# Kernel tuning notes

Measured on AMD Instinct MI355X. Metric: run time of the kernel, lower is better.

## Reference

```python
import jax, jax.numpy as jnp
import numpy as np

D_MODEL = 768
N_HEAD = 12


def setup_inputs() -> dict:
    key = jax.random.key(0)
    k1, k2, k3, k4, k5 = jax.random.split(key, 5)
    B, T, C = 4, 2048, D_MODEL
    s = 1.0 / np.sqrt(C)
    return {
        "x": jax.random.normal(k1, (B, T, C), dtype=jnp.float32),
        "w_attn": jax.random.normal(k2, (C, 3 * C), dtype=jnp.float32) * s,
        "b_attn": jax.random.normal(k3, (3 * C,), dtype=jnp.float32) * 0.02,
        "w_proj": jax.random.normal(k4, (C, C), dtype=jnp.float32) * s,
        "b_proj": jax.random.normal(k5, (C,), dtype=jnp.float32) * 0.02,
    }


def reference(x, w_attn, b_attn, w_proj, b_proj):
    B, T, C = x.shape
    H = N_HEAD
    Dh = C // H
    qkv = x @ w_attn + b_attn                      # [B, T, 3C]
    q, k, v = jnp.split(qkv, 3, axis=-1)
    # [B, H, T, Dh]
    q = q.reshape(B, T, H, Dh).transpose(0, 2, 1, 3)
    k = k.reshape(B, T, H, Dh).transpose(0, 2, 1, 3)
    v = v.reshape(B, T, H, Dh).transpose(0, 2, 1, 3)
    att = jnp.einsum("bhqd,bhkd->bhqk", q, k) * (1.0 / np.sqrt(Dh))
    causal = jnp.tril(jnp.ones((T, T), dtype=bool))
    att = jnp.where(causal[None, None, :, :], att, -jnp.inf)
    att = jax.nn.softmax(att, axis=-1)             # dropout p=0 (eval)
    y = jnp.einsum("bhqk,bhkd->bhqd", att, v)      # [B, H, T, Dh]
    y = y.transpose(0, 2, 1, 3).reshape(B, T, C)
    return y @ w_proj + b_proj
```

## Files before the change

### kernel.cpp

```cpp
#include <hip/hip_runtime.h>
#include <stdint.h>

#define NHEAD 12
#define DH 64
#define BATCH 4
#define SEQ 2048
#define CDIM 768
#define MROWS (BATCH*SEQ)

typedef __attribute__((ext_vector_type(8))) short short8;
typedef __attribute__((ext_vector_type(4))) float floatx4;
typedef unsigned int u32;

__device__ inline unsigned short f2bf(float f) {
    union { float f; unsigned u; } v; v.f = f;
    unsigned r = v.u + 0x7FFFu + ((v.u >> 16) & 1u);
    return (unsigned short)(r >> 16);
}

__device__ __forceinline__ u32 pk_bf16(float a, float b) {
    u32 d;
    asm("v_cvt_pk_bf16_f32 %0, %1, %2" : "=v"(d) : "v"(a), "v"(b));
    return d;
}

__device__ __forceinline__ void async_cp16(const unsigned short* g, unsigned short* l) {
    __builtin_amdgcn_global_load_lds(
        (const __attribute__((address_space(1))) u32*)g,
        (__attribute__((address_space(3))) u32*)l, 16, 0, 0);
}

template<int N> __device__ __forceinline__ void waitcnt_vm() {
    if constexpr (N == 0)      asm volatile("s_waitcnt vmcnt(0)" ::: "memory");
    else if constexpr (N == 3) asm volatile("s_waitcnt vmcnt(3)" ::: "memory");
    else if constexpr (N == 4) asm volatile("s_waitcnt vmcnt(4)" ::: "memory");
}

__device__ __forceinline__ void transpose_tile(
    const float* __restrict__ in, unsigned short* __restrict__ out,
    int K, int N, int k0, int n0, unsigned short (*T)[72]) {
    const int t = threadIdx.x;
    const int nc = t & 63, kw = t >> 6;
    for (int i = 0; i < 16; i++) {
        const int kr = kw + i * 4;
        T[nc][kr] = f2bf(in[(size_t)(k0 + kr) * N + n0 + nc]);
    }
    __syncthreads();
    const int row = t >> 2, seg = t & 3;
    uint4 a = *(const uint4*)&T[row][seg * 16];
    uint4 b2 = *(const uint4*)&T[row][seg * 16 + 8];
    unsigned short* o = &out[(size_t)(n0 + row) * K + k0 + seg * 16];
    *(uint4*)o = a;
    *(uint4*)(o + 8) = b2;
}

__global__ __launch_bounds__(256) void prep_kernel(
    const float* __restrict__ x,      unsigned short* __restrict__ xb,
    const float* __restrict__ wa,     unsigned short* __restrict__ wta,
    const float* __restrict__ wp,     unsigned short* __restrict__ wtp) {
    __shared__ unsigned short T[64][72];
    const int lin = blockIdx.x;
    if (lin < 6144) {
        const int i = (lin * 256 + threadIdx.x) * 4;
        float4 f = *(const float4*)(x + i);
        union { unsigned short s[4]; uint2 u; } p;
        p.s[0] = f2bf(f.x); p.s[1] = f2bf(f.y);
        p.s[2] = f2bf(f.z); p.s[3] = f2bf(f.w);
        *(uint2*)(xb + i) = p.u;
    } else if (lin < 6144 + 432) {
        const int t2 = lin - 6144;
        transpose_tile(wa, wta, CDIM, 3 * CDIM, (t2 % 12) * 64, (t2 / 12) * 64, T);
    } else {
        const int t3 = lin - 6576;
        transpose_tile(wp, wtp, CDIM, CDIM, (t3 % 12) * 64, (t3 / 12) * 64, T);
    }
}

template<int MODE, int KD, int BM, int BN>
__global__ __launch_bounds__(256) void gemm_bf16(
    const unsigned short* __restrict__ A,
    const unsigned short* __restrict__ BT,
    const float* __restrict__ bias,
    float* __restrict__ Cout,
    unsigned short* __restrict__ Qout,
    unsigned short* __restrict__ Kout,
    unsigned short* __restrict__ VTout,
    int Ndim)
{
    constexpr int TM = BM / 32, TN = BN / 32;
    constexpr int CHA = BM / 64, CHB = BN / 64;
    __shared__ unsigned short SH[3 * (BM + BN) * 32];
    auto As = [&](int b3) { return &SH[b3 * BM * 32]; };
    auto Bs = [&](int b3) { return &SH[3 * BM * 32 + b3 * BN * 32]; };

    const int tid  = threadIdx.x;
    const int wave = tid >> 6;
    const int lane = tid & 63;
    const int l16  = lane & 15;
    const int quad = lane >> 4;
    const int wm = wave >> 1, wn = wave & 1;
    const int m0 = blockIdx.x * BM;
    const int n0 = blockIdx.y * BN;

    const int rloc = lane >> 2;
    const int gs   = (((lane & 3) ^ (rloc & 3) ^ ((rloc >> 2) & 3))) * 8;
    const int pg   = ((quad ^ (l16 & 3) ^ ((l16 >> 2) & 3))) * 8;

    floatx4 acc[TM][TN];
    for (int i = 0; i < TM; i++)
        for (int j = 0; j < TN; j++) acc[i][j] = (floatx4)0.0f;

    constexpr int NIT = KD / 32;

    auto stageTo = [&](int s, int buf) {
        const int koff = s * 32;
        for (int ch = 0; ch < CHA; ch++) {
            const int row = wave * CHA * 16 + ch * 16 + rloc;
            async_cp16(&A[(size_t)(m0 + row) * KD + koff + gs],
                       &As(buf)[(wave * CHA + ch) * 512]);
        }
        for (int ch = 0; ch < CHB; ch++) {
            const int row = wave * CHB * 16 + ch * 16 + rloc;
            async_cp16(&BT[(size_t)(n0 + row) * KD + koff + gs],
                       &Bs(buf)[(wave * CHB + ch) * 512]);
        }
    };
    stageTo(0, 0);
    stageTo(1, 1);

    int buf = 0;
    for (int it = 0; it < NIT; it++) {
        if (it < NIT - 1) waitcnt_vm<CHA + CHB>();
        else              waitcnt_vm<0>();
        asm volatile("s_barrier" ::: "memory");
        if (it + 2 < NIT) {
            int b2 = buf + 2; if (b2 >= 3) b2 -= 3;
            stageTo(it + 2, b2);
        }
        short8 a[TM], b[TN];
        for (int i = 0; i < TM; i++)
            a[i] = *(const short8*)&As(buf)[(wm * (BM / 2) + i * 16 + l16) * 32 + pg];
        for (int j = 0; j < TN; j++)
            b[j] = *(const short8*)&Bs(buf)[(wn * (BN / 2) + j * 16 + l16) * 32 + pg];
        for (int i = 0; i < TM; i++)
            for (int j = 0; j < TN; j++)
                acc[i][j] = __builtin_amdgcn_mfma_f32_16x16x32_bf16(
                    a[i], b[j], acc[i][j], 0, 0, 0);
        buf++; if (buf >= 3) buf = 0;
    }

    const float QSCALE = 0.18033688011112042f;

    if (MODE == 1 && (n0 / CDIM) == 2) {
        __syncthreads();
        unsigned short* scr = &SH[wave * (64 * 68)];
        for (int i = 0; i < TM; i++) {
            const int tl = i * 16 + quad * 4;
            for (int j = 0; j < TN; j++) {
                const int dl = j * 16 + l16;
                const float bv = bias[n0 + wn * 64 + j * 16 + l16];
                uint2 u;
                u.x = pk_bf16(acc[i][j][0] + bv, acc[i][j][1] + bv);
                u.y = pk_bf16(acc[i][j][2] + bv, acc[i][j][3] + bv);
                *(uint2*)&scr[dl * 68 + tl] = u;
            }
        }
        const int b_ = m0 >> 11;
        const int tg = (m0 & 2047) + wm * 64;
        const int h  = (n0 - 2 * CDIM + wn * 64) >> 6;
        const size_t rowbase = ((size_t)(b_ * NHEAD + h)) * DH;
        for (int p = 0; p < 8; p++) {
            const int d  = p * 8 + (lane >> 3);
            const int tc = (lane & 7) * 8;
            uint4 v = *(const uint4*)&scr[d * 68 + tc];
            *(uint4*)&VTout[(rowbase + d) * SEQ + tg + tc] = v;
        }
        return;
    }

    for (int i = 0; i < TM; i++) {
        const int mbase = m0 + wm * (BM / 2) + i * 16 + quad * 4;
        for (int j = 0; j < TN; j++) {
            const int ncj  = n0 + wn * (BN / 2) + j * 16;
            const int ncol = ncj + l16;
            const float bv = bias[ncol];
            for (int r = 0; r < 4; r++) {
                const int m = mbase + r;
                const float v = acc[i][j][r] + bv;
                if (MODE == 0) {
                    Cout[(size_t)m * Ndim + ncol] = v;
                } else {
                    const int part = ncj / CDIM;
                    const int c = ncol - part * CDIM;
                    const int hh = c >> 6, d = c & 63;
                    const int b_ = m >> 11, t = m & 2047;
                    const size_t bh = (size_t)(b_ * NHEAD + hh);
                    if (part == 0)
                        Qout[(bh * SEQ + t) * DH + d] = f2bf(v * QSCALE);
                    else
                        Kout[(bh * SEQ + t) * DH + d] = f2bf(v);
                }
            }
        }
    }
}

__global__ __launch_bounds__(256) void attn_kernel(
    const unsigned short* __restrict__ Q,
    const unsigned short* __restrict__ K,
    const unsigned short* __restrict__ VT,
    unsigned short* __restrict__ O)
{
    __shared__ unsigned short Kl[2][2][64 * 32];
    __shared__ unsigned short Vl[2][2][64 * 32];
    __shared__ unsigned short Pl[4][16 * 68];

    const int tid  = threadIdx.x;
    const int wave = tid >> 6;
    const int lane = tid & 63;
    const int l16  = lane & 15;
    const int quad = lane >> 4;

    const int lin = blockIdx.x;
    const int grp = lin >> 3;
    const int xs  = grp & 15;
    const int bh  = ((grp >> 4) << 3) | (lin & 7);
    const int h = bh % NHEAD, b = bh / NHEAD;

    const unsigned short* Qp = Q  + (size_t)bh * SEQ * DH;
    const unsigned short* Kp = K  + (size_t)bh * SEQ * DH;
    const unsigned short* Vp = VT + (size_t)bh * DH * SEQ;

    const int rloc = lane >> 2;
    const int gofsK = ((lane & 3) ^ (rloc & 3) ^ ((rloc >> 2) & 3)) * 8;
    const int pg = ((quad ^ (l16 & 3) ^ ((l16 >> 2) & 3))) * 8;
    const int krow = wave * 16 + rloc;

    for (int pass = 0; pass < 2; pass++) {
        const int qtile = pass == 0 ? xs : 31 - xs;
        const int qb = qtile * 64;
        const int qw = qb + wave * 16;
        const int nkt = qtile + 1;

        short8 aq[2];
        for (int c = 0; c < 2; c++)
            aq[c] = *(const short8*)&Qp[(size_t)(qw + l16) * DH + c * 32 + quad * 8];

        floatx4 accO[4];
        for (int dt = 0; dt < 4; dt++) accO[dt] = (floatx4)0.0f;
        float lp = 0.0f;

        for (int c = 0; c < 2; c++) {
            async_cp16(&Kp[(size_t)krow * DH + c * 32 + gofsK],
                       &Kl[0][c][wave * 512]);
            async_cp16(&Vp[(size_t)krow * SEQ + 0 + c * 32 + gofsK],
                       &Vl[0][c][wave * 512]);
        }

        for (int kt = 0; kt < nkt; kt++) {
            const int kb  = kt * 64;
            const int cur = kt & 1;

            asm volatile("s_waitcnt vmcnt(0)" ::: "memory");
            asm volatile("s_barrier" ::: "memory");

            if (kt + 1 < nkt) {
                const int kbn = kb + 64;
                for (int c = 0; c < 2; c++) {
                    async_cp16(&Kp[(size_t)(kbn + krow) * DH + c * 32 + gofsK],
                               &Kl[cur ^ 1][c][wave * 512]);
                    async_cp16(&Vp[(size_t)krow * SEQ + kbn + c * 32 + gofsK],
                               &Vl[cur ^ 1][c][wave * 512]);
                }
            }

            floatx4 s[4];
            for (int jn = 0; jn < 4; jn++) {
                s[jn] = (floatx4)0.0f;
                for (int c = 0; c < 2; c++) {
                    short8 bk = *(const short8*)
                        &Kl[cur][c][(jn * 16 + l16) * 32 + pg];
                    s[jn] = __builtin_amdgcn_mfma_f32_16x16x32_bf16(
                        bk, aq[c], s[jn], 0, 0, 0);
                }
            }

            if (kt == nkt - 1) {
                const int q = qw + l16;
                for (int jn = 0; jn < 4; jn++) {
                    const int key = kb + jn * 16 + quad * 4;
                    for (int r = 0; r < 4; r++)
                        if (key + r > q) s[jn][r] = -1e30f;
                }
            }

            for (int jn = 0; jn < 4; jn++)
                for (int r = 0; r < 4; r++) {
                    float p = exp2f(s[jn][r]);
                    s[jn][r] = p;
                    lp += p;
                }

            for (int jn = 0; jn < 4; jn++) {
                uint2 u;
                u.x = pk_bf16(s[jn][0], s[jn][1]);
                u.y = pk_bf16(s[jn][2], s[jn][3]);
                *(uint2*)&Pl[wave][l16 * 68 + jn * 16 + quad * 4] = u;
            }
            short8 ap[2];
            for (int c = 0; c < 2; c++) {
                union { short8 v; uint2 u2[2]; } a_;
                const int base = l16 * 68 + c * 32 + quad * 8;
                a_.u2[0] = *(const uint2*)&Pl[wave][base];
                a_.u2[1] = *(const uint2*)&Pl[wave][base + 4];
                ap[c] = a_.v;
            }

            for (int dt = 0; dt < 4; dt++)
                for (int c = 0; c < 2; c++) {
                    short8 bv = *(const short8*)
                        &Vl[cur][c][(dt * 16 + l16) * 32 + pg];
                    accO[dt] = __builtin_amdgcn_mfma_f32_16x16x32_bf16(
                        ap[c], bv, accO[dt], 0, 0, 0);
                }
        }

        float L = lp;
        L += __shfl_xor(L, 16);
        L += __shfl_xor(L, 32);
        for (int r = 0; r < 4; r++) {
            const float Lr = __shfl(L, (lane & 48) | (quad * 4 + r), 64);
            const float inv = 1.0f / Lr;
            const int t = qb + wave * 16 + quad * 4 + r;
            const size_t base = ((size_t)b * SEQ + t) * CDIM + h * DH;
            for (int dt = 0; dt < 4; dt++)
                O[base + dt * 16 + l16] = f2bf(accO[dt][r] * inv);
        }
        __syncthreads();
    }
}

extern "C" void kernel_launch(void* const* d_in, const int* in_sizes, int n_in,
                              void* d_out, int out_size, void* d_ws, size_t ws_size,
                              hipStream_t stream) {
    const float* x      = (const float*)d_in[0];
    const float* w_attn = (const float*)d_in[1];
    const float* b_attn = (const float*)d_in[2];
    const float* w_proj = (const float*)d_in[3];
    const float* b_proj = (const float*)d_in[4];
    float* out = (float*)d_out;

    unsigned short* xb   = (unsigned short*)d_ws;
    unsigned short* wta  = xb  + (size_t)MROWS * CDIM;
    unsigned short* wtp  = wta + (size_t)3 * CDIM * CDIM;
    unsigned short* qws  = wtp + (size_t)CDIM * CDIM;
    unsigned short* kws  = qws + (size_t)MROWS * CDIM;
    unsigned short* vtws = kws + (size_t)MROWS * CDIM;
    unsigned short* ob   = xb;

    prep_kernel<<<6720, 256, 0, stream>>>(x, xb, w_attn, wta, w_proj, wtp);

    dim3 g1(MROWS / 128, (3 * CDIM) / 128);
    gemm_bf16<1, CDIM, 128, 128><<<g1, 256, 0, stream>>>(
        xb, wta, b_attn, nullptr, qws, kws, vtws, 3 * CDIM);

    attn_kernel<<<768, 256, 0, stream>>>(qws, kws, vtws, ob);

    dim3 g3(MROWS / 64, CDIM / 128);
    gemm_bf16<0, CDIM, 64, 128><<<g3, 256, 0, stream>>>(
        ob, wtp, b_proj, out, nullptr, nullptr, nullptr, CDIM);
}
```

Baseline: 207.7 us.

## Restructure attention to 32x32 MFMA with key-split waves and register-resident P

Attention now uses 32x32x16 bf16 MFMAs, and each block handles a single query tile instead of a paired causal pass, so the grid doubles to 1536 blocks launched longest-tile-first. The four waves split into two query groups of 32 rows and two key halves. P stays in registers in the MFMA accumulator layout instead of round-tripping through LDS, and the two key-split partial outputs and row sums are reduced through LDS at the end. This removes the P shared-memory traffic, skips fully masked sub-tiles per wave, and exposes more blocks for load balance. In exchange it adds an end-of-kernel reduction, lowers the per-block work used to balance causal tiles, and brings idle waves on diagonal tiles.

```diff
diff --git a/kernel.cpp b/kernel.cpp
--- a/kernel.cpp
+++ b/kernel.cpp
@@ -10,6 +10,7 @@
 
 typedef __attribute__((ext_vector_type(8))) short short8;
 typedef __attribute__((ext_vector_type(4))) float floatx4;
+typedef __attribute__((ext_vector_type(16))) float floatx16;
 typedef unsigned int u32;
 
 __device__ inline unsigned short f2bf(float f) {
@@ -213,130 +214,133 @@
 {
     __shared__ unsigned short Kl[2][2][64 * 32];
     __shared__ unsigned short Vl[2][2][64 * 32];
-    __shared__ unsigned short Pl[4][16 * 68];
 
     const int tid  = threadIdx.x;
     const int wave = tid >> 6;
     const int lane = tid & 63;
-    const int l16  = lane & 15;
-    const int quad = lane >> 4;
-
-    const int lin = blockIdx.x;
-    const int grp = lin >> 3;
-    const int xs  = grp & 15;
-    const int bh  = ((grp >> 4) << 3) | (lin & 7);
+    const int rl   = lane & 31;
+    const int hi   = lane >> 5;
+    const int qg   = wave >> 1;
+    const int ks   = wave & 1;
+
+    const int idx   = blockIdx.x;
+    const int bh    = idx >> 5;
+    const int qtile = 31 - (idx & 31);
     const int h = bh % NHEAD, b = bh / NHEAD;
+    const int qb = qtile * 64;
 
     const unsigned short* Qp = Q  + (size_t)bh * SEQ * DH;
     const unsigned short* Kp = K  + (size_t)bh * SEQ * DH;
     const unsigned short* Vp = VT + (size_t)bh * DH * SEQ;
 
-    const int rloc = lane >> 2;
+    const int rloc  = lane >> 2;
     const int gofsK = ((lane & 3) ^ (rloc & 3) ^ ((rloc >> 2) & 3)) * 8;
-    const int pg = ((quad ^ (l16 & 3) ^ ((l16 >> 2) & 3))) * 8;
-    const int krow = wave * 16 + rloc;
-
-    for (int pass = 0; pass < 2; pass++) {
-        const int qtile = pass == 0 ? xs : 31 - xs;
-        const int qb = qtile * 64;
-        const int qw = qb + wave * 16;
-        const int nkt = qtile + 1;
-
-        short8 aq[2];
-        for (int c = 0; c < 2; c++)
-            aq[c] = *(const short8*)&Qp[(size_t)(qw + l16) * DH + c * 32 + quad * 8];
-
-        floatx4 accO[4];
-        for (int dt = 0; dt < 4; dt++) accO[dt] = (floatx4)0.0f;
-        float lp = 0.0f;
-
+    const int krow  = wave * 16 + rloc;
+    const int swz   = (rl & 3) ^ ((rl >> 2) & 3);
+
+    short8 aq[4];
+#pragma unroll
+    for (int dc = 0; dc < 4; dc++)
+        aq[dc] = *(const short8*)&Qp[(size_t)(qb + qg * 32 + rl) * DH + dc * 16 + hi * 8];
+
+    floatx16 accO[2];
+    accO[0] = (floatx16)0.0f;
+    accO[1] = (floatx16)0.0f;
+    float lp = 0.0f;
+
+    const int nkt = qtile + 1;
+
+    auto stage = [&](int kt, int bufb) {
+#pragma unroll
         for (int c = 0; c < 2; c++) {
-            async_cp16(&Kp[(size_t)krow * DH + c * 32 + gofsK],
-                       &Kl[0][c][wave * 512]);
-            async_cp16(&Vp[(size_t)krow * SEQ + 0 + c * 32 + gofsK],
-                       &Vl[0][c][wave * 512]);
-        }
-
-        for (int kt = 0; kt < nkt; kt++) {
-            const int kb  = kt * 64;
-            const int cur = kt & 1;
-
-            asm volatile("s_waitcnt vmcnt(0)" ::: "memory");
-            asm volatile("s_barrier" ::: "memory");
-
-            if (kt + 1 < nkt) {
-                const int kbn = kb + 64;
-                for (int c = 0; c < 2; c++) {
-                    async_cp16(&Kp[(size_t)(kbn + krow) * DH + c * 32 + gofsK],
-                               &Kl[cur ^ 1][c][wave * 512]);
-                    async_cp16(&Vp[(size_t)krow * SEQ + kbn + c * 32 + gofsK],
-                               &Vl[cur ^ 1][c][wave * 512]);
+            async_cp16(&Kp[(size_t)(kt * 64 + krow) * DH + c * 32 + gofsK],
+                       &Kl[bufb][c][wave * 512]);
+            async_cp16(&Vp[(size_t)krow * SEQ + kt * 64 + c * 32 + gofsK],
+                       &Vl[bufb][c][wave * 512]);
+        }
+    };
+
+    stage(0, 0);
+
+    for (int kt = 0; kt < nkt; kt++) {
+        const int cur = kt & 1;
+        asm volatile("s_waitcnt vmcnt(0)" ::: "memory");
+        asm volatile("s_barrier" ::: "memory");
+        if (kt + 1 < nkt) stage(kt + 1, cur ^ 1);
+
+        const int kq = (kt - qtile) * 64 + (ks - qg) * 32;
+        if (kq <= 0) {
+            floatx16 s = (floatx16)0.0f;
+#pragma unroll
+            for (int dc = 0; dc < 4; dc++) {
+                const int p = (((dc & 1) * 2 + hi) ^ swz);
+                const short8 ak = *(const short8*)
+                    &Kl[cur][dc >> 1][(ks * 32 + rl) * 32 + p * 8];
+                s = __builtin_amdgcn_mfma_f32_32x32x16_bf16(ak, aq[dc], s, 0, 0, 0);
+            }
+            if (kq == 0) {
+#pragma unroll
+                for (int r = 0; r < 16; r++) {
+                    const int kl = (r & 3) + 8 * (r >> 2) + 4 * hi;
+                    if (kl > rl) s[r] = -1e30f;
                 }
             }
-
-            floatx4 s[4];
-            for (int jn = 0; jn < 4; jn++) {
-                s[jn] = (floatx4)0.0f;
-                for (int c = 0; c < 2; c++) {
-                    short8 bk = *(const short8*)
-                        &Kl[cur][c][(jn * 16 + l16) * 32 + pg];
-                    s[jn] = __builtin_amdgcn_mfma_f32_16x16x32_bf16(
-                        bk, aq[c], s[jn], 0, 0, 0);
+            float pe[16];
+#pragma unroll
+            for (int r = 0; r < 16; r++) { pe[r] = exp2f(s[r]); lp += pe[r]; }
+            u32 u[8];
+#pragma unroll
+            for (int i = 0; i < 8; i++) u[i] = pk_bf16(pe[2 * i], pe[2 * i + 1]);
+
+#pragma unroll
+            for (int ksl = 0; ksl < 2; ksl++) {
+                union { short8 v; u32 w[4]; } pa;
+                pa.w[0] = u[4 * ksl + 0]; pa.w[1] = u[4 * ksl + 1];
+                pa.w[2] = u[4 * ksl + 2]; pa.w[3] = u[4 * ksl + 3];
+                const int p1 = (2 * ksl) ^ swz;
+#pragma unroll
+                for (int db = 0; db < 2; db++) {
+                    const int drow = db * 32 + rl;
+                    union { short8 v; u32 w[4]; } bv;
+                    const uint2 v1 = *(const uint2*)
+                        &Vl[cur][ks][drow * 32 + p1 * 8 + hi * 4];
+                    const uint2 v2 = *(const uint2*)
+                        &Vl[cur][ks][drow * 32 + (p1 ^ 1) * 8 + hi * 4];
+                    bv.w[0] = v1.x; bv.w[1] = v1.y; bv.w[2] = v2.x; bv.w[3] = v2.y;
+                    accO[db] = __builtin_amdgcn_mfma_f32_32x32x16_bf16(
+                        pa.v, bv.v, accO[db], 0, 0, 0);
                 }
             }
-
-            if (kt == nkt - 1) {
-                const int q = qw + l16;
-                for (int jn = 0; jn < 4; jn++) {
-                    const int key = kb + jn * 16 + quad * 4;
-                    for (int r = 0; r < 4; r++)
-                        if (key + r > q) s[jn][r] = -1e30f;
-                }
-            }
-
-            for (int jn = 0; jn < 4; jn++)
-                for (int r = 0; r < 4; r++) {
-                    float p = exp2f(s[jn][r]);
-                    s[jn][r] = p;
-                    lp += p;
-                }
-
-            for (int jn = 0; jn < 4; jn++) {
-                uint2 u;
-                u.x = pk_bf16(s[jn][0], s[jn][1]);
-                u.y = pk_bf16(s[jn][2], s[jn][3]);
-                *(uint2*)&Pl[wave][l16 * 68 + jn * 16 + quad * 4] = u;
-            }
-            short8 ap[2];
-            for (int c = 0; c < 2; c++) {
-                union { short8 v; uint2 u2[2]; } a_;
-                const int base = l16 * 68 + c * 32 + quad * 8;
-                a_.u2[0] = *(const uint2*)&Pl[wave][base];
-                a_.u2[1] = *(const uint2*)&Pl[wave][base + 4];
-                ap[c] = a_.v;
-            }
-
-            for (int dt = 0; dt < 4; dt++)
-                for (int c = 0; c < 2; c++) {
-                    short8 bv = *(const short8*)
-                        &Vl[cur][c][(dt * 16 + l16) * 32 + pg];
-                    accO[dt] = __builtin_amdgcn_mfma_f32_16x16x32_bf16(
-                        ap[c], bv, accO[dt], 0, 0, 0);
-                }
-        }
-
-        float L = lp;
-        L += __shfl_xor(L, 16);
-        L += __shfl_xor(L, 32);
-        for (int r = 0; r < 4; r++) {
-            const float Lr = __shfl(L, (lane & 48) | (quad * 4 + r), 64);
-            const float inv = 1.0f / Lr;
-            const int t = qb + wave * 16 + quad * 4 + r;
+        }
+    }
+
+    float Lw = lp + __shfl_xor(lp, 32);
+    __syncthreads();
+    float* redO = (float*)&Kl[0][0][0];
+    float* redL = (float*)&Vl[0][0][0];
+    if (ks == 1) {
+#pragma unroll
+        for (int db = 0; db < 2; db++)
+#pragma unroll
+            for (int r = 0; r < 16; r++)
+                redO[(qg * 32 + db * 16 + r) * 64 + lane] = accO[db][r];
+        if (hi == 0) redL[qg * 32 + rl] = Lw;
+    }
+    __syncthreads();
+    if (ks == 0) {
+        const float inv = 1.0f / (Lw + redL[qg * 32 + rl]);
+#pragma unroll
+        for (int r = 0; r < 16; r++) {
+            const int qrow = (r & 3) + 8 * (r >> 2) + 4 * hi;
+            const float iv = __shfl(inv, qrow, 64);
+            const int t = qb + qg * 32 + qrow;
             const size_t base = ((size_t)b * SEQ + t) * CDIM + h * DH;
-            for (int dt = 0; dt < 4; dt++)
-                O[base + dt * 16 + l16] = f2bf(accO[dt][r] * inv);
-        }
-        __syncthreads();
+#pragma unroll
+            for (int db = 0; db < 2; db++) {
+                const float o = accO[db][r] + redO[(qg * 32 + db * 16 + r) * 64 + lane];
+                O[base + db * 32 + rl] = f2bf(o * iv);
+            }
+        }
     }
 }
 
@@ -364,7 +368,7 @@
     gemm_bf16<1, CDIM, 128, 128><<<g1, 256, 0, stream>>>(
         xb, wta, b_attn, nullptr, qws, kws, vtws, 3 * CDIM);
 
-    attn_kernel<<<768, 256, 0, stream>>>(qws, kws, vtws, ob);
+    attn_kernel<<<1536, 256, 0, stream>>>(qws, kws, vtws, ob);
 
     dim3 g3(MROWS / 64, CDIM / 128);
     gemm_bf16<0, CDIM, 64, 128><<<g3, 256, 0, stream>>>(
```

New measurement: 263.8 us. 27.0% more time.
